# Performance work log

Measured on AMD Instinct MI355X. Metric: run time of the kernel, lower is better.

Reference implementation:

```python
import jax, jax.numpy as jnp
import numpy as np

N_NODES = 100_000
N_EDGES = 3_200_000


def setup_inputs() -> dict:
    key = jax.random.key(0)
    ks = jax.random.split(key, 13)
    x_node = jax.random.normal(ks[0], (N_NODES, 32), jnp.float32)
    x_edge = jax.random.normal(ks[1], (N_EDGES, 6), jnp.float32)
    src = jax.random.randint(ks[2], (N_EDGES,), 0, N_NODES)
    dst = jax.random.randint(ks[3], (N_EDGES,), 0, N_NODES)
    b_mask = jax.random.randint(ks[4], (N_EDGES,), 0, 2).astype(jnp.int32)
    s = 0.1  # small init scale for numerical sanity
    Wn1 = jax.random.normal(ks[5], (38, 64), jnp.float32) * s
    bn1 = jax.random.normal(ks[6], (64,), jnp.float32) * s
    Wn2 = jax.random.normal(ks[7], (64, 32), jnp.float32) * s
    bn2 = jax.random.normal(ks[8], (32,), jnp.float32) * s
    We1 = jax.random.normal(ks[9], (70, 32), jnp.float32) * s
    be1 = jax.random.normal(ks[10], (32,), jnp.float32) * s
    We2 = jax.random.normal(ks[11], (32, 6), jnp.float32) * s
    be2 = jax.random.normal(ks[12], (6,), jnp.float32) * s
    return dict(x_node=x_node, x_edge=x_edge, src=src, dst=dst, b_mask=b_mask,
                Wn1=Wn1, bn1=bn1, Wn2=Wn2, bn2=bn2,
                We1=We1, be1=be1, We2=We2, be2=be2)


def reference(x_node, x_edge, src, dst, b_mask,
              Wn1, bn1, Wn2, bn2, We1, be1, We2, be2):
    # Edge messages: forward edges (b_mask==0) use [src, dst, e];
    # backward edges (b_mask==1) use [dst, src, e]. One fused pass.
    back = (b_mask == 1)[:, None]
    xs = x_node[src]                      # [E, 32]
    xd = x_node[dst]                      # [E, 32]
    a = jnp.where(back, xd, xs)
    b = jnp.where(back, xs, xd)
    feat_e = jnp.concatenate([a, b, x_edge], axis=1)          # [E, 70]
    em = jax.nn.relu(feat_e @ We1 + be1) @ We2 + be2          # [E, 6]

    # Node messages: per in-edge, MLP([dst_x, em]); sum into dst node.
    feat_n = jnp.concatenate([xd, em], axis=1)                # [E, 38]
    msg = jax.nn.relu(feat_n @ Wn1 + bn1) @ Wn2 + bn2         # [E, 32]
    nm = jax.ops.segment_sum(msg, dst, num_segments=x_node.shape[0])  # [N, 32]
    return nm, em
```

## Files before the change

kernel.cpp:

```cpp
#include <hip/hip_runtime.h>
#include <hip/hip_bf16.h>

typedef __attribute__((ext_vector_type(8))) short short8;
typedef __attribute__((ext_vector_type(4))) float f32x4;
typedef __attribute__((ext_vector_type(2))) float f32x2;

#define NN 100000
#define NE 3200000
#define NTILES (NE / 16)

__device__ __forceinline__ short f2bf(float f) {
  __hip_bfloat16 h = __float2bfloat16(f);
  return *reinterpret_cast<short*>(&h);
}

__device__ __forceinline__ f32x4 mfma16(short8 a, short8 b, f32x4 c) {
  return __builtin_amdgcn_mfma_f32_16x16x32_bf16(a, b, c, 0, 0, 0);
}

__global__ void __launch_bounds__(256) mpn_main(
    const float* __restrict__ x_node,
    const float* __restrict__ x_edge,
    const int*   __restrict__ srcp,
    const int*   __restrict__ dstp,
    const int*   __restrict__ bmp,
    const float* __restrict__ Wn1, const float* __restrict__ bn1,
    const float* __restrict__ Wn2, const float* __restrict__ bn2,
    const float* __restrict__ We1, const float* __restrict__ be1,
    const float* __restrict__ We2, const float* __restrict__ be2,
    float* __restrict__ out_nm,
    float* __restrict__ out_em)
{
  __shared__ short lds_h1[4][16][40];
  __shared__ float lds_em[4][16][12];
  __shared__ short lds_h2[4][16][72];

  const int tid  = threadIdx.x;
  const int wid  = tid >> 6;
  const int lane = tid & 63;
  const int col  = lane & 15;
  const int kg   = lane >> 4;

  for (int i = lane; i < 16 * 12; i += 64)
    ((float*)lds_em[wid])[i] = 0.f;

  auto ldb = [&](const float* W, int K, int N, int kc, int nt) {
    int n  = nt * 16 + col;
    int k0 = kc * 32 + kg * 8;
    short8 r;
#pragma unroll
    for (int j = 0; j < 8; ++j) {
      int k = k0 + j;
      float v = (k < K && n < N) ? W[k * N + n] : 0.f;
      r[j] = f2bf(v);
    }
    return r;
  };

  short8 B_e1[3][2], B_n1[2][4], B_n2[2][2], B_e2;
#pragma unroll
  for (int kc = 0; kc < 3; ++kc)
#pragma unroll
    for (int nt = 0; nt < 2; ++nt) B_e1[kc][nt] = ldb(We1, 70, 32, kc, nt);
  B_e2 = ldb(We2, 32, 6, 0, 0);
#pragma unroll
  for (int kc = 0; kc < 2; ++kc)
#pragma unroll
    for (int nt = 0; nt < 4; ++nt) B_n1[kc][nt] = ldb(Wn1, 38, 64, kc, nt);
#pragma unroll
  for (int kc = 0; kc < 2; ++kc)
#pragma unroll
    for (int nt = 0; nt < 2; ++nt) B_n2[kc][nt] = ldb(Wn2, 64, 32, kc, nt);

  float bias_e1[2], bias_n1[4], bias_n2[2], bias_e2;
  bias_e1[0] = be1[col];      bias_e1[1] = be1[16 + col];
  bias_e2    = (col < 6) ? be2[col] : 0.f;
#pragma unroll
  for (int nt = 0; nt < 4; ++nt) bias_n1[nt] = bn1[nt * 16 + col];
  bias_n2[0] = bn2[col];      bias_n2[1] = bn2[16 + col];

  const int gw = blockIdx.x * 4 + wid;
  const int nw = gridDim.x * 4;
  if (gw >= NTILES) return;

  auto ldidx = [&](int t, int& s, int& d, int& b) {
    int e = t * 16 + col;
    s = srcp[e]; d = dstp[e]; b = bmp[e];
  };
  auto gather = [&](int t, int s, int d,
                    f32x4& g0, f32x4& g1, f32x4& g2, f32x4& g3,
                    f32x2& e0, f32x2& e1, f32x2& e2) {
    const float* ps = x_node + (long)s * 32 + kg * 8;
    const float* pd = x_node + (long)d * 32 + kg * 8;
    g0 = *(const f32x4*)ps; g1 = *(const f32x4*)(ps + 4);
    g2 = *(const f32x4*)pd; g3 = *(const f32x4*)(pd + 4);
    if (kg == 0) {
      const float* pe = x_edge + (long)(t * 16 + col) * 6;
      e0 = *(const f32x2*)pe; e1 = *(const f32x2*)(pe + 2); e2 = *(const f32x2*)(pe + 4);
    }
  };

  int sI, dI, bI;
  int tC = gw;
  ldidx(tC, sI, dI, bI);
  f32x4 Rs0, Rs1, Rd0, Rd1; f32x2 Re0, Re1, Re2;
  gather(tC, sI, dI, Rs0, Rs1, Rd0, Rd1, Re0, Re1, Re2);
  int bR = bI;
  int tN = gw + nw;
  { int tc = (tN < NTILES) ? tN : (NTILES - 1); ldidx(tc, sI, dI, bI); }

  while (true) {
    f32x4 Ns0, Ns1, Nd0, Nd1; f32x2 Ne0, Ne1, Ne2;
    { int tc = (tN < NTILES) ? tN : (NTILES - 1);
      gather(tc, sI, dI, Ns0, Ns1, Nd0, Nd1, Ne0, Ne1, Ne2); }
    int bN = bI;
    { int t2 = tN + nw; int tc = (t2 < NTILES) ? t2 : (NTILES - 1);
      ldidx(tc, sI, dI, bI); }

    const int eb = tC * 16;
    int de[4];
#pragma unroll
    for (int r = 0; r < 4; ++r) de[r] = dstp[eb + kg * 4 + r];

    short8 XS, XD;
#pragma unroll
    for (int j = 0; j < 4; ++j) {
      XS[j] = f2bf(Rs0[j]); XS[4 + j] = f2bf(Rs1[j]);
      XD[j] = f2bf(Rd0[j]); XD[4 + j] = f2bf(Rd1[j]);
    }
    short8 AE = {0, 0, 0, 0, 0, 0, 0, 0};
    if (kg == 0) {
      AE[0] = f2bf(Re0[0]); AE[1] = f2bf(Re0[1]);
      AE[2] = f2bf(Re1[0]); AE[3] = f2bf(Re1[1]);
      AE[4] = f2bf(Re2[0]); AE[5] = f2bf(Re2[1]);
    }
    const bool back = (bR != 0);
    short8 Aa = back ? XD : XS;
    short8 Ab = back ? XS : XD;

    f32x4 a0 = {bias_e1[0], bias_e1[0], bias_e1[0], bias_e1[0]};
    f32x4 a1 = {bias_e1[1], bias_e1[1], bias_e1[1], bias_e1[1]};
    a0 = mfma16(Aa, B_e1[0][0], a0);
    a0 = mfma16(Ab, B_e1[1][0], a0);
    a0 = mfma16(AE, B_e1[2][0], a0);
    a1 = mfma16(Aa, B_e1[0][1], a1);
    a1 = mfma16(Ab, B_e1[1][1], a1);
    a1 = mfma16(AE, B_e1[2][1], a1);

#pragma unroll
    for (int r = 0; r < 4; ++r) {
      lds_h1[wid][kg * 4 + r][col]      = f2bf(fmaxf(a0[r], 0.f));
      lds_h1[wid][kg * 4 + r][16 + col] = f2bf(fmaxf(a1[r], 0.f));
    }
    short8 Ah1 = *(const short8*)&lds_h1[wid][col][kg * 8];

    f32x4 ae2 = {bias_e2, bias_e2, bias_e2, bias_e2};
    ae2 = mfma16(Ah1, B_e2, ae2);

    if (col < 6) {
#pragma unroll
      for (int r = 0; r < 4; ++r) {
        int row = kg * 4 + r;
        float v = ae2[r];
        out_em[(long)(eb + row) * 6 + col] = v;
        lds_em[wid][row][col] = v;
      }
    }
    short8 Aem = {0, 0, 0, 0, 0, 0, 0, 0};
    if (kg == 0) {
      f32x4 u0 = *(const f32x4*)&lds_em[wid][col][0];
      f32x4 u1 = *(const f32x4*)&lds_em[wid][col][4];
      Aem[0] = f2bf(u0[0]); Aem[1] = f2bf(u0[1]);
      Aem[2] = f2bf(u0[2]); Aem[3] = f2bf(u0[3]);
      Aem[4] = f2bf(u1[0]); Aem[5] = f2bf(u1[1]);
      Aem[6] = f2bf(u1[2]); Aem[7] = f2bf(u1[3]);
    }

    f32x4 an[4];
#pragma unroll
    for (int nt = 0; nt < 4; ++nt) {
      an[nt] = (f32x4){bias_n1[nt], bias_n1[nt], bias_n1[nt], bias_n1[nt]};
      an[nt] = mfma16(XD,  B_n1[0][nt], an[nt]);
      an[nt] = mfma16(Aem, B_n1[1][nt], an[nt]);
    }
#pragma unroll
    for (int nt = 0; nt < 4; ++nt)
#pragma unroll
      for (int r = 0; r < 4; ++r)
        lds_h2[wid][kg * 4 + r][nt * 16 + col] = f2bf(fmaxf(an[nt][r], 0.f));
    short8 Ah2a = *(const short8*)&lds_h2[wid][col][kg * 8];
    short8 Ah2b = *(const short8*)&lds_h2[wid][col][32 + kg * 8];

    f32x4 am0 = {bias_n2[0], bias_n2[0], bias_n2[0], bias_n2[0]};
    f32x4 am1 = {bias_n2[1], bias_n2[1], bias_n2[1], bias_n2[1]};
    am0 = mfma16(Ah2a, B_n2[0][0], am0);
    am0 = mfma16(Ah2b, B_n2[1][0], am0);
    am1 = mfma16(Ah2a, B_n2[0][1], am1);
    am1 = mfma16(Ah2b, B_n2[1][1], am1);

#pragma unroll
    for (int r = 0; r < 4; ++r) {
      float* basep = out_nm + (long)de[r] * 32 + col;
      unsafeAtomicAdd(basep,      am0[r]);
      unsafeAtomicAdd(basep + 16, am1[r]);
    }

    tC = tN; tN += nw;
    if (tC >= NTILES) break;
    Rs0 = Ns0; Rs1 = Ns1; Rd0 = Nd0; Rd1 = Nd1;
    Re0 = Ne0; Re1 = Ne1; Re2 = Ne2;
    bR = bN;
  }
}

extern "C" void kernel_launch(void* const* d_in, const int* in_sizes, int n_in,
                              void* d_out, int out_size, void* d_ws, size_t ws_size,
                              hipStream_t stream) {
  const float* x_node = (const float*)d_in[0];
  const float* x_edge = (const float*)d_in[1];
  const int*   src    = (const int*)d_in[2];
  const int*   dst    = (const int*)d_in[3];
  const int*   bm     = (const int*)d_in[4];
  const float* Wn1 = (const float*)d_in[5];  const float* bn1 = (const float*)d_in[6];
  const float* Wn2 = (const float*)d_in[7];  const float* bn2 = (const float*)d_in[8];
  const float* We1 = (const float*)d_in[9];  const float* be1 = (const float*)d_in[10];
  const float* We2 = (const float*)d_in[11]; const float* be2 = (const float*)d_in[12];
  float* out_nm = (float*)d_out;
  float* out_em = out_nm + (size_t)NN * 32;

  hipMemsetAsync(out_nm, 0, (size_t)NN * 32 * sizeof(float), stream);
  mpn_main<<<2048, 256, 0, stream>>>(x_node, x_edge, src, dst, bm,
                                     Wn1, bn1, Wn2, bn2, We1, be1, We2, be2,
                                     out_nm, out_em);
}
```

Measured before the change: 354.0 us.

## Sort edges by destination and reduce messages per node before atomics

Adds a counting sort of edges by destination (histogram, three-pass scan, scatter) run each call, then has each wave process a contiguous block of sorted tiles. Messages sharing a destination are summed in registers through LDS, so global atomics are issued once per run of equal destinations instead of once per edge. The cost is five extra kernel launches plus atomic-heavy histogram and scatter passes, and the gathers of x_edge, src and the out_em writes become indirect and scattered. The sort runs every call, so this is legitimate per-call work.

```diff
diff --git a/kernel.cpp b/kernel.cpp
--- a/kernel.cpp
+++ b/kernel.cpp
@@ -8,6 +8,9 @@
 #define NN 100000
 #define NE 3200000
 #define NTILES (NE / 16)
+#define NBLK_SCAN 391
+#define NWAVES 8192
+#define KTILES 25
 
 __device__ __forceinline__ short f2bf(float f) {
   __hip_bfloat16 h = __float2bfloat16(f);
@@ -16,6 +19,62 @@
 
 __device__ __forceinline__ f32x4 mfma16(short8 a, short8 b, f32x4 c) {
   return __builtin_amdgcn_mfma_f32_16x16x32_bf16(a, b, c, 0, 0, 0);
+}
+
+__global__ void __launch_bounds__(256) k_hist(const int* __restrict__ dst,
+                                              int* __restrict__ counts) {
+  int i = blockIdx.x * 256 + threadIdx.x;
+  if (i < NE) atomicAdd(&counts[dst[i]], 1);
+}
+
+__global__ void __launch_bounds__(256) k_scan1(const int* __restrict__ counts,
+                                               int* __restrict__ loff,
+                                               int* __restrict__ blocksum) {
+  __shared__ int sm[256];
+  int t = threadIdx.x;
+  int i = blockIdx.x * 256 + t;
+  int v = (i < NN) ? counts[i] : 0;
+  sm[t] = v; __syncthreads();
+  for (int off = 1; off < 256; off <<= 1) {
+    int x = (t >= off) ? sm[t - off] : 0;
+    __syncthreads();
+    sm[t] += x;
+    __syncthreads();
+  }
+  if (i < NN) loff[i] = sm[t] - v;
+  if (t == 255) blocksum[blockIdx.x] = sm[255];
+}
+
+__global__ void __launch_bounds__(512) k_scan2(const int* __restrict__ blocksum,
+                                               int* __restrict__ blockpref) {
+  __shared__ int sm[512];
+  int t = threadIdx.x;
+  int v = (t < NBLK_SCAN) ? blocksum[t] : 0;
+  sm[t] = v; __syncthreads();
+  for (int off = 1; off < 512; off <<= 1) {
+    int x = (t >= off) ? sm[t - off] : 0;
+    __syncthreads();
+    sm[t] += x;
+    __syncthreads();
+  }
+  if (t < NBLK_SCAN) blockpref[t] = sm[t] - v;
+}
+
+__global__ void __launch_bounds__(256) k_scan3(const int* __restrict__ loff,
+                                               const int* __restrict__ blockpref,
+                                               int* __restrict__ cursor) {
+  int i = blockIdx.x * 256 + threadIdx.x;
+  if (i < NN) cursor[i] = loff[i] + blockpref[blockIdx.x];
+}
+
+__global__ void __launch_bounds__(256) k_scatter(const int* __restrict__ dst,
+                                                 int* __restrict__ cursor,
+                                                 int* __restrict__ sorted) {
+  int i = blockIdx.x * 256 + threadIdx.x;
+  if (i < NE) {
+    int p = atomicAdd(&cursor[dst[i]], 1);
+    sorted[p] = i;
+  }
 }
 
 __global__ void __launch_bounds__(256) mpn_main(
@@ -24,6 +83,7 @@
     const int*   __restrict__ srcp,
     const int*   __restrict__ dstp,
     const int*   __restrict__ bmp,
+    const int*   __restrict__ sorted,
     const float* __restrict__ Wn1, const float* __restrict__ bn1,
     const float* __restrict__ Wn2, const float* __restrict__ bn2,
     const float* __restrict__ We1, const float* __restrict__ be1,
@@ -34,6 +94,9 @@
   __shared__ short lds_h1[4][16][40];
   __shared__ float lds_em[4][16][12];
   __shared__ short lds_h2[4][16][72];
+  __shared__ float lds_ms[4][16][33];
+  __shared__ int   lds_eid[4][16];
+  __shared__ int   lds_dst[4][16];
 
   const int tid  = threadIdx.x;
   const int wid  = tid >> 6;
@@ -80,14 +143,15 @@
   bias_n2[0] = bn2[col];      bias_n2[1] = bn2[16 + col];
 
   const int gw = blockIdx.x * 4 + wid;
-  const int nw = gridDim.x * 4;
-  if (gw >= NTILES) return;
-
-  auto ldidx = [&](int t, int& s, int& d, int& b) {
-    int e = t * 16 + col;
+  const int t0 = gw * KTILES;
+  const int tE = min(t0 + KTILES, NTILES);
+  if (t0 >= NTILES) return;
+
+  auto ldidx = [&](int t, int& e, int& s, int& d, int& b) {
+    e = sorted[t * 16 + col];
     s = srcp[e]; d = dstp[e]; b = bmp[e];
   };
-  auto gather = [&](int t, int s, int d,
+  auto gather = [&](int e, int s, int d,
                     f32x4& g0, f32x4& g1, f32x4& g2, f32x4& g3,
                     f32x2& e0, f32x2& e1, f32x2& e2) {
     const float* ps = x_node + (long)s * 32 + kg * 8;
@@ -95,32 +159,31 @@
     g0 = *(const f32x4*)ps; g1 = *(const f32x4*)(ps + 4);
     g2 = *(const f32x4*)pd; g3 = *(const f32x4*)(pd + 4);
     if (kg == 0) {
-      const float* pe = x_edge + (long)(t * 16 + col) * 6;
+      const float* pe = x_edge + (long)e * 6;
       e0 = *(const f32x2*)pe; e1 = *(const f32x2*)(pe + 2); e2 = *(const f32x2*)(pe + 4);
     }
   };
 
-  int sI, dI, bI;
-  int tC = gw;
-  ldidx(tC, sI, dI, bI);
+  float accL  = 0.f;
+  int   curDst = -1;
+
+  int eI, sI, dI, bI;
+  int tC = t0;
+  ldidx(tC, eI, sI, dI, bI);
   f32x4 Rs0, Rs1, Rd0, Rd1; f32x2 Re0, Re1, Re2;
-  gather(tC, sI, dI, Rs0, Rs1, Rd0, Rd1, Re0, Re1, Re2);
-  int bR = bI;
-  int tN = gw + nw;
-  { int tc = (tN < NTILES) ? tN : (NTILES - 1); ldidx(tc, sI, dI, bI); }
+  gather(eI, sI, dI, Rs0, Rs1, Rd0, Rd1, Re0, Re1, Re2);
+  int bR = bI, eR = eI, dR = dI;
+  int tN = t0 + 1;
+  { int tc = (tN < tE) ? tN : (tE - 1); ldidx(tc, eI, sI, dI, bI); }
 
   while (true) {
     f32x4 Ns0, Ns1, Nd0, Nd1; f32x2 Ne0, Ne1, Ne2;
-    { int tc = (tN < NTILES) ? tN : (NTILES - 1);
-      gather(tc, sI, dI, Ns0, Ns1, Nd0, Nd1, Ne0, Ne1, Ne2); }
-    int bN = bI;
-    { int t2 = tN + nw; int tc = (t2 < NTILES) ? t2 : (NTILES - 1);
-      ldidx(tc, sI, dI, bI); }
-
-    const int eb = tC * 16;
-    int de[4];
-#pragma unroll
-    for (int r = 0; r < 4; ++r) de[r] = dstp[eb + kg * 4 + r];
+    gather(eI, sI, dI, Ns0, Ns1, Nd0, Nd1, Ne0, Ne1, Ne2);
+    int bN = bI, eN = eI, dN = dI;
+    { int t2 = tN + 1; int tc = (t2 < tE) ? t2 : (tE - 1);
+      ldidx(tc, eI, sI, dI, bI); }
+
+    if (kg == 0) { lds_eid[wid][col] = eR; lds_dst[wid][col] = dR; }
 
     short8 XS, XD;
 #pragma unroll
@@ -162,7 +225,7 @@
       for (int r = 0; r < 4; ++r) {
         int row = kg * 4 + r;
         float v = ae2[r];
-        out_em[(long)(eb + row) * 6 + col] = v;
+        out_em[(long)lds_eid[wid][row] * 6 + col] = v;
         lds_em[wid][row][col] = v;
       }
     }
@@ -200,17 +263,34 @@
 
 #pragma unroll
     for (int r = 0; r < 4; ++r) {
-      float* basep = out_nm + (long)de[r] * 32 + col;
-      unsafeAtomicAdd(basep,      am0[r]);
-      unsafeAtomicAdd(basep + 16, am1[r]);
-    }
-
-    tC = tN; tN += nw;
-    if (tC >= NTILES) break;
+      lds_ms[wid][kg * 4 + r][col]      = am0[r];
+      lds_ms[wid][kg * 4 + r][16 + col] = am1[r];
+    }
+    if (lane < 32) {
+#pragma unroll
+      for (int r = 0; r < 16; ++r) {
+        int   dr = lds_dst[wid][r];
+        float v  = lds_ms[wid][r][lane];
+        if (dr != curDst) {
+          if (curDst >= 0)
+            unsafeAtomicAdd(out_nm + (long)curDst * 32 + lane, accL);
+          curDst = dr;
+          accL = v;
+        } else {
+          accL += v;
+        }
+      }
+    }
+
+    tC = tN; tN += 1;
+    if (tC >= tE) break;
     Rs0 = Ns0; Rs1 = Ns1; Rd0 = Nd0; Rd1 = Nd1;
     Re0 = Ne0; Re1 = Ne1; Re2 = Ne2;
-    bR = bN;
+    bR = bN; eR = eN; dR = dN;
   }
+
+  if (lane < 32 && curDst >= 0)
+    unsafeAtomicAdd(out_nm + (long)curDst * 32 + lane, accL);
 }
 
 extern "C" void kernel_launch(void* const* d_in, const int* in_sizes, int n_in,
@@ -228,8 +308,24 @@
   float* out_nm = (float*)d_out;
   float* out_em = out_nm + (size_t)NN * 32;
 
+  int* ws        = (int*)d_ws;
+  int* counts    = ws;
+  int* loff      = ws + 100000;
+  int* blocksum  = ws + 200000;
+  int* blockpref = ws + 200512;
+  int* cursor    = ws + 201024;
+  int* sorted    = ws + 301024;
+
+  hipMemsetAsync(counts, 0, (size_t)NN * sizeof(int), stream);
   hipMemsetAsync(out_nm, 0, (size_t)NN * 32 * sizeof(float), stream);
-  mpn_main<<<2048, 256, 0, stream>>>(x_node, x_edge, src, dst, bm,
+
+  k_hist<<<(NE + 255) / 256, 256, 0, stream>>>(dst, counts);
+  k_scan1<<<NBLK_SCAN, 256, 0, stream>>>(counts, loff, blocksum);
+  k_scan2<<<1, 512, 0, stream>>>(blocksum, blockpref);
+  k_scan3<<<NBLK_SCAN, 256, 0, stream>>>(loff, blockpref, cursor);
+  k_scatter<<<(NE + 255) / 256, 256, 0, stream>>>(dst, cursor, sorted);
+
+  mpn_main<<<2048, 256, 0, stream>>>(x_node, x_edge, src, dst, bm, sorted,
                                      Wn1, bn1, Wn2, bn2, We1, be1, We2, be2,
                                      out_nm, out_em);
 }
```

Result: slower. 866.0 us (+144.6%).
